# Optimization experiments

Measured on AMD Instinct MI355X. Metric: run time of the kernel, lower is better.

Reference implementation:

```python
import jax, jax.numpy as jnp
import numpy as np

B, S, D, H = 2, 2048, 1024, 16
HD = D // H  # head size 64

def setup_inputs() -> dict:
    key = jax.random.key(0)
    ks = jax.random.split(key, 7)
    sc = 1.0 / np.sqrt(D)
    return {
        "batch_data": jax.random.normal(ks[0], (B, S, D), dtype=jnp.float32),
        "Wq": jax.random.normal(ks[1], (D, D), dtype=jnp.float32) * sc,
        "bq": jnp.zeros((D,), dtype=jnp.float32),
        "Wk": jax.random.normal(ks[2], (D, D), dtype=jnp.float32) * sc,
        "bk": jnp.zeros((D,), dtype=jnp.float32),
        "Wv": jax.random.normal(ks[3], (D, D), dtype=jnp.float32) * sc,
        "bv": jnp.zeros((D,), dtype=jnp.float32),
    }

def _split_heads(x):
    # [B,S,D] -> [B,H,S,HD]
    b, s, _ = x.shape
    return x.reshape(b, s, H, HD).transpose(0, 2, 1, 3)

def reference(batch_data, Wq, bq, Wk, bk, Wv, bv):
    q = _split_heads(batch_data @ Wq + bq)
    k = _split_heads(batch_data @ Wk + bk)
    v = _split_heads(batch_data @ Wv + bv)
    scores = jnp.einsum('bhqd,bhkd->bhqk', q, k) / jnp.sqrt(jnp.float32(HD))
    probs = jax.nn.softmax(scores, axis=-1)
    ctx = jnp.einsum('bhqk,bhkd->bhqd', probs, v)  # [B,H,S,HD]
    ctx = ctx.transpose(0, 2, 1, 3).reshape(batch_data.shape[0], batch_data.shape[1], D)
    return jnp.mean(ctx, axis=1)  # mean pool over sequence -> [B,D]
```

## Files before the change

kernel.cpp:

```cpp
#include <hip/hip_runtime.h>
#include <hip/hip_bf16.h>
#include <stdint.h>

#define B_  2
#define S_  2048
#define D_  1024
#define H_  16
#define HD_ 64

typedef __attribute__((ext_vector_type(8)))  __bf16 bf16x8;
typedef __attribute__((ext_vector_type(4)))  __bf16 bf16x4;
typedef __attribute__((ext_vector_type(2)))  __bf16 bf16x2;
typedef __attribute__((ext_vector_type(4)))  float  f32x4;
typedef __attribute__((ext_vector_type(16))) float  f32x16;
typedef __attribute__((ext_vector_type(4)))  uint32_t u32x4;

#define QSCALE 0.18033688011112042f

__device__ __forceinline__ void gload16(const void* g, void* l) {
  __builtin_amdgcn_global_load_lds(
      (__attribute__((address_space(1))) void*)(uintptr_t)g,
      (__attribute__((address_space(3))) void*)(uintptr_t)l,
      16, 0, 0);
}

__global__ __launch_bounds__(256) void prep(
    const float* __restrict__ x, const float* __restrict__ wq,
    const float* __restrict__ wk, const float* __restrict__ wv,
    __bf16* __restrict__ xb, __bf16* __restrict__ wt, float* __restrict__ out) {
  __shared__ float tile[32][33];
  const int t = threadIdx.x;
  const int bx = blockIdx.x;
  if (bx < 4096) {
    int i = bx * 256 + t;
    float4 v = ((const float4*)x)[i];
    bf16x4 o;
    o[0] = (__bf16)v.x; o[1] = (__bf16)v.y; o[2] = (__bf16)v.z; o[3] = (__bf16)v.w;
    ((bf16x4*)xb)[i] = o;
  } else if (bx < 7168) {
    int tb = bx - 4096;
    int z = tb >> 10;
    int rem = tb & 1023;
    int n0 = (rem & 31) * 32, k0 = (rem >> 5) * 32;
    const float* w = (z == 0) ? wq : (z == 1 ? wk : wv);
    __bf16* o = wt + (size_t)z * D_ * D_;
    int tx = t & 31, ty = t >> 5;
    for (int i = 0; i < 4; ++i)
      tile[ty + 8 * i][tx] = w[(size_t)(k0 + ty + 8 * i) * D_ + n0 + tx];
    __syncthreads();
    for (int i = 0; i < 4; ++i)
      o[(size_t)(n0 + ty + 8 * i) * D_ + k0 + tx] = (__bf16)tile[tx][ty + 8 * i];
  } else {
    float4* o4 = (float4*)out;
    float4 z4 = {0.f, 0.f, 0.f, 0.f};
    o4[t] = z4;
    o4[t + 256] = z4;
  }
}

__global__ __launch_bounds__(256, 3) void gemm_qkv(
    const __bf16* __restrict__ xb, const __bf16* __restrict__ wt,
    const float* __restrict__ bq, const float* __restrict__ bk,
    const float* __restrict__ bv, __bf16* __restrict__ qh,
    __bf16* __restrict__ kh, __bf16* __restrict__ vt) {
  constexpr int K = 1024;
  constexpr int NIT = K / 32;
  __shared__ __attribute__((aligned(16))) __bf16 lA[2][128 * 32];
  __shared__ __attribute__((aligned(16))) __bf16 lB[2][128 * 32];

  const int z = blockIdx.z;
  const __bf16* w = wt + (size_t)z * K * D_;
  const float* bias = (z == 0) ? bq : (z == 1 ? bk : bv);
  const int t = threadIdx.x;
  const int lane = t & 63;
  const int wid = t >> 6;
  const int quad = lane >> 4;
  const int col = lane & 15;
  const int m0 = blockIdx.x * 128;
  const int n0 = blockIdx.y * 128;
  const int wr = (wid >> 1) * 64;
  const int wc = (wid & 1) * 64;

  const int sr0 = t >> 2;
  const int gc = (t & 3) ^ ((t >> 2) & 3);

  auto stage = [&](int kt, int buf) {
    gload16(xb + (size_t)(m0 + sr0) * K + kt * 32 + gc * 8,
            (char*)&lA[buf][0] + t * 16);
    gload16(xb + (size_t)(m0 + 64 + sr0) * K + kt * 32 + gc * 8,
            (char*)&lA[buf][0] + 4096 + t * 16);
    gload16(w + (size_t)(n0 + sr0) * K + kt * 32 + gc * 8,
            (char*)&lB[buf][0] + t * 16);
    gload16(w + (size_t)(n0 + 64 + sr0) * K + kt * 32 + gc * 8,
            (char*)&lB[buf][0] + 4096 + t * 16);
  };

  f32x4 acc[4][4] = {};

  stage(0, 0);

  if (z < 2) {
    for (int kt = 0; kt < NIT; ++kt) {
      const int cur = kt & 1;
      __syncthreads();
      if (kt + 1 < NIT) stage(kt + 1, cur ^ 1);
      bf16x8 fw[4], fx[4];
      for (int i = 0; i < 4; ++i) {
        int n = wr + i * 16 + col;
        int sl = quad ^ (n & 3);
        fw[i] = *(const bf16x8*)((const char*)&lB[cur][0] + n * 64 + sl * 16);
      }
      for (int j = 0; j < 4; ++j) {
        int m = wc + j * 16 + col;
        int sl = quad ^ (m & 3);
        fx[j] = *(const bf16x8*)((const char*)&lA[cur][0] + m * 64 + sl * 16);
      }
      for (int i = 0; i < 4; ++i)
        for (int j = 0; j < 4; ++j)
          acc[i][j] = __builtin_amdgcn_mfma_f32_16x16x32_bf16(
              fw[i], fx[j], acc[i][j], 0, 0, 0);
    }
    const float scale = (z == 0) ? QSCALE : 1.0f;
    __bf16* dst = (z == 0) ? qh : kh;
    for (int i = 0; i < 4; ++i) {
      int gnb = n0 + wr + i * 16 + quad * 4;
      float4 bi = *(const float4*)(bias + gnb);
      int h = gnb >> 6, hd = gnb & 63;
      for (int j = 0; j < 4; ++j) {
        int gm = m0 + wc + j * 16 + col;
        int b = gm >> 11, s = gm & 2047;
        bf16x4 pk;
        pk[0] = (__bf16)((acc[i][j][0] + bi.x) * scale);
        pk[1] = (__bf16)((acc[i][j][1] + bi.y) * scale);
        pk[2] = (__bf16)((acc[i][j][2] + bi.z) * scale);
        pk[3] = (__bf16)((acc[i][j][3] + bi.w) * scale);
        *(bf16x4*)(dst + ((size_t)(b * H_ + h) * S_ + s) * HD_ + hd) = pk;
      }
    }
  } else {
    for (int kt = 0; kt < NIT; ++kt) {
      const int cur = kt & 1;
      __syncthreads();
      if (kt + 1 < NIT) stage(kt + 1, cur ^ 1);
      bf16x8 fx[4], fw[4];
      for (int i = 0; i < 4; ++i) {
        int m = wr + i * 16 + col;
        int sl = quad ^ (m & 3);
        fx[i] = *(const bf16x8*)((const char*)&lA[cur][0] + m * 64 + sl * 16);
      }
      for (int j = 0; j < 4; ++j) {
        int n = wc + j * 16 + col;
        int sl = quad ^ (n & 3);
        fw[j] = *(const bf16x8*)((const char*)&lB[cur][0] + n * 64 + sl * 16);
      }
      for (int i = 0; i < 4; ++i)
        for (int j = 0; j < 4; ++j)
          acc[i][j] = __builtin_amdgcn_mfma_f32_16x16x32_bf16(
              fx[i], fw[j], acc[i][j], 0, 0, 0);
    }
    for (int i = 0; i < 4; ++i) {
      int gmb = m0 + wr + i * 16 + quad * 4;
      int b = gmb >> 11, s = gmb & 2047;
      for (int j = 0; j < 4; ++j) {
        int gn = n0 + wc + j * 16 + col;
        int h = gn >> 6, hd = gn & 63;
        float bi = bias[gn];
        bf16x4 pk;
        pk[0] = (__bf16)(acc[i][j][0] + bi);
        pk[1] = (__bf16)(acc[i][j][1] + bi);
        pk[2] = (__bf16)(acc[i][j][2] + bi);
        pk[3] = (__bf16)(acc[i][j][3] + bi);
        *(bf16x4*)(vt + ((size_t)(b * H_ + h) * HD_ + hd) * S_ + s) = pk;
      }
    }
  }
}

__global__ __launch_bounds__(256, 4) void attn1(
    const __bf16* __restrict__ qh, const __bf16* __restrict__ kh,
    const __bf16* __restrict__ vt, __bf16* __restrict__ po,
    float* __restrict__ pl) {
  __shared__ __attribute__((aligned(16))) __bf16 lK[128 * 64];
  __shared__ __attribute__((aligned(16))) __bf16 lV[64 * 128];

  const int t = threadIdx.x;
  const int lane = t & 63;
  const int half = lane >> 5;
  const int q31 = lane & 31;
  const int bh = blockIdx.x;
  const int kc = blockIdx.z;
  const int q0w = blockIdx.y * 128 + (t >> 6) * 32;

  const __bf16* qbase = qh + (size_t)bh * S_ * HD_;
  const __bf16* kbase = kh + (size_t)bh * S_ * HD_;
  const __bf16* vbase = vt + (size_t)bh * HD_ * S_;

  bf16x8 aq[4];
  for (int ks = 0; ks < 4; ++ks)
    aq[ks] = *(const bf16x8*)(qbase + (size_t)(q0w + q31) * HD_ + ks * 16 + half * 8);

  f32x16 o[2] = {};
  float lsum = 0.f;

  const int kgc = (t & 7) ^ ((t >> 3) & 7);
  const int vgc = (t & 15) ^ ((t >> 4) & 15);

  for (int kt = kc * 8; kt < kc * 8 + 8; ++kt) {
    __syncthreads();
    for (int r = 0; r < 4; ++r) {
      int row = r * 32 + (t >> 3);
      gload16(kbase + (size_t)(kt * 128 + row) * HD_ + kgc * 8,
              (char*)lK + r * 4096 + t * 16);
      int rowv = r * 16 + (t >> 4);
      gload16(vbase + (size_t)rowv * S_ + kt * 128 + vgc * 8,
              (char*)lV + r * 4096 + t * 16);
    }
    __syncthreads();

    for (int st = 0; st < 4; ++st) {
      f32x16 sc = {};
      for (int ks = 0; ks < 4; ++ks) {
        int row = st * 32 + q31;
        int ch = (ks * 2 + half) ^ (row & 7);
        bf16x8 fk = *(const bf16x8*)((const char*)lK + row * 128 + ch * 16);
        sc = __builtin_amdgcn_mfma_f32_32x32x16_bf16(fk, aq[ks], sc, 0, 0, 0);
      }

      uint32_t pk[8], x[8];
      for (int p = 0; p < 8; ++p) {
        float ea = __builtin_amdgcn_exp2f(sc[2 * p]);
        float eb = __builtin_amdgcn_exp2f(sc[2 * p + 1]);
        lsum += ea;
        lsum += eb;
        uint32_t au = __builtin_bit_cast(uint32_t, ea) + 0x8000u;
        uint32_t bu = __builtin_bit_cast(uint32_t, eb) + 0x8000u;
        pk[p] = __builtin_amdgcn_perm(bu, au, 0x07060302u);
      }
      for (int p = 0; p < 8; ++p) x[p] = __shfl_xor((int)pk[p], 32);

      bool h1 = (half != 0);
      u32x4 f0 = {h1 ? x[2] : pk[0], h1 ? x[3] : pk[1],
                  h1 ? pk[2] : x[0], h1 ? pk[3] : x[1]};
      u32x4 f1 = {h1 ? x[6] : pk[4], h1 ? x[7] : pk[5],
                  h1 ? pk[6] : x[4], h1 ? pk[7] : x[5]};
      bf16x8 Fa = __builtin_bit_cast(bf16x8, f0);
      bf16x8 Fb = __builtin_bit_cast(bf16x8, f1);

      for (int hdt = 0; hdt < 2; ++hdt) {
        int rowv = hdt * 32 + q31;
        int ch0 = (st * 4 + half) ^ (rowv & 15);
        int ch1 = (st * 4 + 2 + half) ^ (rowv & 15);
        bf16x8 fv0 = *(const bf16x8*)((const char*)lV + rowv * 256 + ch0 * 16);
        bf16x8 fv1 = *(const bf16x8*)((const char*)lV + rowv * 256 + ch1 * 16);
        o[hdt] = __builtin_amdgcn_mfma_f32_32x32x16_bf16(fv0, Fa, o[hdt], 0, 0, 0);
        o[hdt] = __builtin_amdgcn_mfma_f32_32x32x16_bf16(fv1, Fb, o[hdt], 0, 0, 0);
      }
    }
  }

  float ltot = lsum + __shfl_xor(lsum, 32);
  const size_t slab = (size_t)(kc * 32 + bh) * S_;
  const int qrow = q0w + q31;
  if (half == 0) pl[slab + qrow] = ltot;
  for (int hdt = 0; hdt < 2; ++hdt)
    for (int rq = 0; rq < 4; ++rq) {
      bf16x4 pk;
      pk[0] = (__bf16)o[hdt][rq * 4 + 0];
      pk[1] = (__bf16)o[hdt][rq * 4 + 1];
      pk[2] = (__bf16)o[hdt][rq * 4 + 2];
      pk[3] = (__bf16)o[hdt][rq * 4 + 3];
      *(bf16x4*)(po + (slab + qrow) * HD_ + hdt * 32 + rq * 8 + half * 4) = pk;
    }
}

__global__ __launch_bounds__(256) void attn2(const __bf16* __restrict__ po,
                                             const float* __restrict__ pl,
                                             float* __restrict__ out) {
  __shared__ float red[256];
  const int t = threadIdx.x;
  const int hd = t & 63;
  const int rgrp = t >> 6;
  const int bh = blockIdx.y;
  const int r0 = blockIdx.x * 256 + rgrp * 64;
  const size_t s0 = (size_t)bh * S_;
  const size_t s1 = (size_t)(32 + bh) * S_;
  float acc = 0.f;
  for (int i = 0; i < 64; ++i) {
    int row = r0 + i;
    float l = pl[s0 + row] + pl[s1 + row];
    float v = (float)po[(s0 + row) * HD_ + hd] +
              (float)po[(s1 + row) * HD_ + hd];
    acc += v / l;
  }
  red[t] = acc;
  __syncthreads();
  if (t < 64) {
    float s = red[t] + red[t + 64] + red[t + 128] + red[t + 192];
    atomicAdd(out + (size_t)(bh >> 4) * D_ + (bh & 15) * HD_ + hd,
              s * (1.0f / S_));
  }
}

extern "C" void kernel_launch(void* const* d_in, const int* in_sizes, int n_in,
                              void* d_out, int out_size, void* d_ws, size_t ws_size,
                              hipStream_t stream) {
  const float* x  = (const float*)d_in[0];
  const float* Wq = (const float*)d_in[1];
  const float* bq = (const float*)d_in[2];
  const float* Wk = (const float*)d_in[3];
  const float* bk = (const float*)d_in[4];
  const float* Wv = (const float*)d_in[5];
  const float* bv = (const float*)d_in[6];
  float* out = (float*)d_out;

  char* ws = (char*)d_ws;
  __bf16* qh = (__bf16*)(ws);
  __bf16* kh = (__bf16*)(ws + ((size_t)8  << 20));
  __bf16* vt = (__bf16*)(ws + ((size_t)16 << 20));
  __bf16* xb = (__bf16*)(ws + ((size_t)24 << 20));
  __bf16* wt = (__bf16*)(ws + ((size_t)32 << 20));
  __bf16* po = (__bf16*)(ws + ((size_t)24 << 20));
  float*  pl = (float*) (ws + ((size_t)40 << 20));

  prep<<<dim3(7169), dim3(256), 0, stream>>>(x, Wq, Wk, Wv, xb, wt, out);
  gemm_qkv<<<dim3(32, 8, 3), dim3(256), 0, stream>>>(xb, wt, bq, bk, bv, qh, kh, vt);
  attn1<<<dim3(B_ * H_, S_ / 128, 2), dim3(256), 0, stream>>>(qh, kh, vt, po, pl);
  attn2<<<dim3(8, B_ * H_), dim3(256), 0, stream>>>(po, pl, out);
}
```

Before: 169.0 us.

## Double-buffer K/V tiles and use K8 MFMA to avoid lane shuffles

The attention kernel now loads 64-key K/V tiles into two LDS buffers, prefetching the next tile while computing the current one. This replaces the previous load-then-compute pattern with two barriers per 128-key tile. When the 32x32x8 bf16 MFMA builtin exists, the P·V product feeds the exp-packed probabilities straight into K=8 MFMAs, which removes the cross-half __shfl_xor permutation but issues twice as many smaller MFMAs. Only one barrier per iteration remains. Correctness depends on the async global-to-LDS loads being complete at that barrier, and no explicit wait is visible.

```diff
diff --git a/kernel.cpp b/kernel.cpp
--- a/kernel.cpp
+++ b/kernel.cpp
@@ -11,11 +11,19 @@
 typedef __attribute__((ext_vector_type(8)))  __bf16 bf16x8;
 typedef __attribute__((ext_vector_type(4)))  __bf16 bf16x4;
 typedef __attribute__((ext_vector_type(2)))  __bf16 bf16x2;
+typedef __attribute__((ext_vector_type(4)))  short  s16x4;
 typedef __attribute__((ext_vector_type(4)))  float  f32x4;
 typedef __attribute__((ext_vector_type(16))) float  f32x16;
+typedef __attribute__((ext_vector_type(2)))  uint32_t u32x2;
 typedef __attribute__((ext_vector_type(4)))  uint32_t u32x4;
 
 #define QSCALE 0.18033688011112042f
+
+#if __has_builtin(__builtin_amdgcn_mfma_f32_32x32x8bf16_1k)
+#define HAVE_MFMA_K8 1
+#else
+#define HAVE_MFMA_K8 0
+#endif
 
 __device__ __forceinline__ void gload16(const void* g, void* l) {
   __builtin_amdgcn_global_load_lds(
@@ -180,8 +188,8 @@
     const __bf16* __restrict__ qh, const __bf16* __restrict__ kh,
     const __bf16* __restrict__ vt, __bf16* __restrict__ po,
     float* __restrict__ pl) {
-  __shared__ __attribute__((aligned(16))) __bf16 lK[128 * 64];
-  __shared__ __attribute__((aligned(16))) __bf16 lV[64 * 128];
+  __shared__ __attribute__((aligned(16))) __bf16 lK[2][64 * 64];
+  __shared__ __attribute__((aligned(16))) __bf16 lV[2][64 * 64];
 
   const int t = threadIdx.x;
   const int lane = t & 63;
@@ -202,31 +210,37 @@
   f32x16 o[2] = {};
   float lsum = 0.f;
 
-  const int kgc = (t & 7) ^ ((t >> 3) & 7);
-  const int vgc = (t & 15) ^ ((t >> 4) & 15);
-
-  for (int kt = kc * 8; kt < kc * 8 + 8; ++kt) {
+  const int srow = t >> 3;
+  const int sgc = (t & 7) ^ (srow & 7);
+
+  auto stage = [&](int kt, int buf) {
+    gload16(kbase + (size_t)(kt * 64 + srow) * HD_ + sgc * 8,
+            (char*)&lK[buf][0] + t * 16);
+    gload16(kbase + (size_t)(kt * 64 + 32 + srow) * HD_ + sgc * 8,
+            (char*)&lK[buf][0] + 4096 + t * 16);
+    gload16(vbase + (size_t)srow * S_ + kt * 64 + sgc * 8,
+            (char*)&lV[buf][0] + t * 16);
+    gload16(vbase + (size_t)(32 + srow) * S_ + kt * 64 + sgc * 8,
+            (char*)&lV[buf][0] + 4096 + t * 16);
+  };
+
+  stage(kc * 16, 0);
+
+  for (int kt0 = 0; kt0 < 16; ++kt0) {
+    const int cur = kt0 & 1;
     __syncthreads();
-    for (int r = 0; r < 4; ++r) {
-      int row = r * 32 + (t >> 3);
-      gload16(kbase + (size_t)(kt * 128 + row) * HD_ + kgc * 8,
-              (char*)lK + r * 4096 + t * 16);
-      int rowv = r * 16 + (t >> 4);
-      gload16(vbase + (size_t)rowv * S_ + kt * 128 + vgc * 8,
-              (char*)lV + r * 4096 + t * 16);
-    }
-    __syncthreads();
-
-    for (int st = 0; st < 4; ++st) {
+    if (kt0 + 1 < 16) stage(kc * 16 + kt0 + 1, cur ^ 1);
+
+    for (int st = 0; st < 2; ++st) {
       f32x16 sc = {};
+      const int row = st * 32 + q31;
       for (int ks = 0; ks < 4; ++ks) {
-        int row = st * 32 + q31;
-        int ch = (ks * 2 + half) ^ (row & 7);
-        bf16x8 fk = *(const bf16x8*)((const char*)lK + row * 128 + ch * 16);
+        int pos = (2 * ks + half) ^ (row & 7);
+        bf16x8 fk = *(const bf16x8*)((const char*)&lK[cur][0] + row * 128 + pos * 16);
         sc = __builtin_amdgcn_mfma_f32_32x32x16_bf16(fk, aq[ks], sc, 0, 0, 0);
       }
 
-      uint32_t pk[8], x[8];
+      uint32_t pk[8];
       for (int p = 0; p < 8; ++p) {
         float ea = __builtin_amdgcn_exp2f(sc[2 * p]);
         float eb = __builtin_amdgcn_exp2f(sc[2 * p + 1]);
@@ -236,8 +250,22 @@
         uint32_t bu = __builtin_bit_cast(uint32_t, eb) + 0x8000u;
         pk[p] = __builtin_amdgcn_perm(bu, au, 0x07060302u);
       }
+
+#if HAVE_MFMA_K8
+      for (int hdt = 0; hdt < 2; ++hdt) {
+        const int rowv = hdt * 32 + q31;
+        for (int g = 0; g < 4; ++g) {
+          int pos = (4 * st + g) ^ (rowv & 7);
+          s16x4 fv = *(const s16x4*)((const char*)&lV[cur][0] + rowv * 128 +
+                                     pos * 16 + half * 8);
+          u32x2 fpu = {pk[2 * g], pk[2 * g + 1]};
+          s16x4 fp = __builtin_bit_cast(s16x4, fpu);
+          o[hdt] = __builtin_amdgcn_mfma_f32_32x32x8bf16_1k(fv, fp, o[hdt], 0, 0, 0);
+        }
+      }
+#else
+      uint32_t x[8];
       for (int p = 0; p < 8; ++p) x[p] = __shfl_xor((int)pk[p], 32);
-
       bool h1 = (half != 0);
       u32x4 f0 = {h1 ? x[2] : pk[0], h1 ? x[3] : pk[1],
                   h1 ? pk[2] : x[0], h1 ? pk[3] : x[1]};
@@ -245,16 +273,16 @@
                   h1 ? pk[6] : x[4], h1 ? pk[7] : x[5]};
       bf16x8 Fa = __builtin_bit_cast(bf16x8, f0);
       bf16x8 Fb = __builtin_bit_cast(bf16x8, f1);
-
       for (int hdt = 0; hdt < 2; ++hdt) {
-        int rowv = hdt * 32 + q31;
-        int ch0 = (st * 4 + half) ^ (rowv & 15);
-        int ch1 = (st * 4 + 2 + half) ^ (rowv & 15);
-        bf16x8 fv0 = *(const bf16x8*)((const char*)lV + rowv * 256 + ch0 * 16);
-        bf16x8 fv1 = *(const bf16x8*)((const char*)lV + rowv * 256 + ch1 * 16);
+        const int rowv = hdt * 32 + q31;
+        int ch0 = (4 * st + half) ^ (rowv & 7);
+        int ch1 = (4 * st + 2 + half) ^ (rowv & 7);
+        bf16x8 fv0 = *(const bf16x8*)((const char*)&lV[cur][0] + rowv * 128 + ch0 * 16);
+        bf16x8 fv1 = *(const bf16x8*)((const char*)&lV[cur][0] + rowv * 128 + ch1 * 16);
         o[hdt] = __builtin_amdgcn_mfma_f32_32x32x16_bf16(fv0, Fa, o[hdt], 0, 0, 0);
         o[hdt] = __builtin_amdgcn_mfma_f32_32x32x16_bf16(fv1, Fb, o[hdt], 0, 0, 0);
       }
+#endif
     }
   }
 
```

Measured after the change: 172.7 us. +2.2%, slower.
